# Performance work log

Measured on AMD Instinct MI355X. Metric: run time of the kernel, lower is better.

Reference implementation:

```python
import jax, jax.numpy as jnp
import numpy as np

D = 512
H = 8
HD = D // H
EPS = 1e-6


def layer_norm(x, a, b):
    # torch: std is unbiased (ddof=1); note division by (std + eps), not sqrt(var+eps)
    mean = x.mean(-1, keepdims=True)
    std = jnp.sqrt(x.var(-1, ddof=1, keepdims=True))
    return a * (x - mean) / (std + EPS) + b


def setup_inputs() -> dict:
    key = jax.random.key(0)
    ks = jax.random.split(key, 8)
    x = jax.random.normal(ks[0], (4, 2048, D), dtype=jnp.float32)
    s = 0.02
    return {
        "x": x,
        "ln1_a": jnp.ones((D,), jnp.float32),
        "ln1_b": jnp.zeros((D,), jnp.float32),
        "ln2_a": jnp.ones((D,), jnp.float32),
        "ln2_b": jnp.zeros((D,), jnp.float32),
        "wq": jax.random.normal(ks[1], (D, D), jnp.float32) * s,  # [out, in] torch layout
        "wk": jax.random.normal(ks[2], (D, D), jnp.float32) * s,
        "wv": jax.random.normal(ks[3], (D, D), jnp.float32) * s,
        "wo": jax.random.normal(ks[4], (D, D), jnp.float32) * s,
        "w1": jax.random.normal(ks[5], (D, D), jnp.float32) * s,  # MLP hidden == dim
        "b1": jnp.zeros((D,), jnp.float32),
        "w2": jax.random.normal(ks[6], (D, D), jnp.float32) * s,
        "b2": jnp.zeros((D,), jnp.float32),
    }


def reference(x, ln1_a, ln1_b, ln2_a, ln2_b, wq, wk, wv, wo, w1, b1, w2, b2):
    B, S, _ = x.shape
    xn = layer_norm(x, ln1_a, ln1_b)
    # attention (non-causal, dropout=identity in eval)
    q = (xn @ wq.T).reshape(B, S, H, HD)
    k = (xn @ wk.T).reshape(B, S, H, HD)
    v = (xn @ wv.T).reshape(B, S, H, HD)
    scores = jnp.einsum("bshd,bthd->bhst", q, k) / jnp.sqrt(jnp.float32(HD))
    probs = jax.nn.softmax(scores.astype(jnp.float32), axis=-1).astype(q.dtype)
    attn = jnp.einsum("bhst,bthd->bshd", probs, v).reshape(B, S, D)
    h = xn + attn @ wo.T
    # MLP
    hn = layer_norm(h, ln2_a, ln2_b)
    ffn = jax.nn.relu(hn @ w1.T + b1) @ w2.T + b2
    return h + ffn
```

## Files before the change

### kernel.cpp

```cpp
#include <hip/hip_runtime.h>


typedef short s16x8 __attribute__((ext_vector_type(8)));
typedef float f32x4 __attribute__((ext_vector_type(4)));
typedef unsigned short u16;
typedef u16 u16x4 __attribute__((ext_vector_type(4)));

__device__ __forceinline__ u16 f2b(float f) {
  union { float f; unsigned u; } c; c.f = f;
  return (u16)((c.u + 0x7FFFu + ((c.u >> 16) & 1u)) >> 16);
}

__device__ __forceinline__ f32x4 mfma16(s16x8 a, s16x8 b, f32x4 c) {
  return __builtin_amdgcn_mfma_f32_16x16x32_bf16(a, b, c, 0, 0, 0);
}

__device__ __forceinline__ void gload_lds16(const u16* g, u16* l) {
  __builtin_amdgcn_global_load_lds(
      (const __attribute__((address_space(1))) unsigned*)g,
      (__attribute__((address_space(3))) unsigned*)l, 16, 0, 0);
}

__global__ __launch_bounds__(256) void cast_w(
    const float* __restrict__ s0, const float* __restrict__ s1,
    const float* __restrict__ s2, const float* __restrict__ s3,
    const float* __restrict__ s4, const float* __restrict__ s5,
    u16* __restrict__ dst)
{
  int i = blockIdx.x * 256 + threadIdx.x;
  const float* s;
  switch (blockIdx.y) {
    case 0: s = s0; break; case 1: s = s1; break; case 2: s = s2; break;
    case 3: s = s3; break; case 4: s = s4; break; default: s = s5; break;
  }
  float4 v = ((const float4*)s)[i];
  u16x4 o; o.x = f2b(v.x); o.y = f2b(v.y); o.z = f2b(v.z); o.w = f2b(v.w);
  *(u16x4*)(dst + (size_t)blockIdx.y * 262144 + (size_t)i * 4) = o;
}

template<int OF, int OB>
__global__ __launch_bounds__(256) void ln_kernel(
    const float* __restrict__ x, const float* __restrict__ ga,
    const float* __restrict__ gbv, float* __restrict__ yf, u16* __restrict__ yb)
{
  int row = blockIdx.x * 4 + (threadIdx.x >> 6);
  int lane = threadIdx.x & 63;
  size_t base = (size_t)row * 512 + lane * 8;
  const float4* xr = (const float4*)(x + base);
  float4 v0 = xr[0], v1 = xr[1];
  float s  = v0.x + v0.y + v0.z + v0.w + v1.x + v1.y + v1.z + v1.w;
  float ss = v0.x*v0.x + v0.y*v0.y + v0.z*v0.z + v0.w*v0.w
           + v1.x*v1.x + v1.y*v1.y + v1.z*v1.z + v1.w*v1.w;
  #pragma unroll
  for (int m = 1; m < 64; m <<= 1) { s += __shfl_xor(s, m); ss += __shfl_xor(ss, m); }
  float mean = s * (1.0f / 512.0f);
  float var  = fmaxf((ss - 512.0f * mean * mean) * (1.0f / 511.0f), 0.0f);
  float inv  = 1.0f / (sqrtf(var) + 1e-6f);
  const float4* ap = (const float4*)(ga + lane * 8);
  const float4* bp = (const float4*)(gbv + lane * 8);
  float4 a0 = ap[0], a1 = ap[1], b0 = bp[0], b1 = bp[1];
  float4 y0, y1;
  y0.x = (v0.x-mean)*inv*a0.x + b0.x;  y0.y = (v0.y-mean)*inv*a0.y + b0.y;
  y0.z = (v0.z-mean)*inv*a0.z + b0.z;  y0.w = (v0.w-mean)*inv*a0.w + b0.w;
  y1.x = (v1.x-mean)*inv*a1.x + b1.x;  y1.y = (v1.y-mean)*inv*a1.y + b1.y;
  y1.z = (v1.z-mean)*inv*a1.z + b1.z;  y1.w = (v1.w-mean)*inv*a1.w + b1.w;
  if (OF) { float4* o = (float4*)(yf + base); o[0] = y0; o[1] = y1; }
  if (OB) {
    union { s16x8 v; u16 u[8]; } pk;
    pk.u[0]=f2b(y0.x); pk.u[1]=f2b(y0.y); pk.u[2]=f2b(y0.z); pk.u[3]=f2b(y0.w);
    pk.u[4]=f2b(y1.x); pk.u[5]=f2b(y1.y); pk.u[6]=f2b(y1.z); pk.u[7]=f2b(y1.w);
    *(s16x8*)(yb + base) = pk.v;
  }
}

template<int MODE>
__global__ __launch_bounds__(256) void gemm128(
    const u16* __restrict__ A, const u16* __restrict__ W,
    const float* __restrict__ bias, const float* __restrict__ resid,
    float* __restrict__ outf, u16* __restrict__ outb,
    u16* __restrict__ outb3, float qscale)
{
  __shared__ u16 als[2][128 * 32];
  __shared__ u16 bls[2][128 * 32];
  int t = threadIdx.x, lane = t & 63, w = t >> 6;
  int l15 = lane & 15, g = lane >> 4;
  int wr = w >> 1, wc = w & 1;
  int mbase = blockIdx.x * 128, nbase = blockIdx.y * 128;

  int r0 = t >> 2, cs = (t & 3) ^ ((r0 >> 1) & 3);
  size_t offA0 = (size_t)(mbase + r0) * 512 + cs * 8;
  size_t offA1 = (size_t)(mbase + r0 + 64) * 512 + cs * 8;
  size_t offB0 = (size_t)(nbase + r0) * 512 + cs * 8;
  size_t offB1 = (size_t)(nbase + r0 + 64) * 512 + cs * 8;

  #define GSTAGE(buf, k0) do {                                    \
    gload_lds16(A + (k0) + offA0, &als[buf][(w * 64) * 8]);       \
    gload_lds16(A + (k0) + offA1, &als[buf][(256 + w * 64) * 8]); \
    gload_lds16(W + (k0) + offB0, &bls[buf][(w * 64) * 8]);       \
    gload_lds16(W + (k0) + offB1, &bls[buf][(256 + w * 64) * 8]); \
  } while (0)

  int ar[4], br[4];
  #pragma unroll
  for (int i = 0; i < 4; ++i) {
    int rA = wr * 64 + i * 16 + l15;
    ar[i] = rA * 32 + ((g ^ ((rA >> 1) & 3)) << 3);
    int rB = wc * 64 + i * 16 + l15;
    br[i] = rB * 32 + ((g ^ ((rB >> 1) & 3)) << 3);
  }

  f32x4 zero = {0.0f, 0.0f, 0.0f, 0.0f};
  f32x4 acc[4][4];
  #pragma unroll
  for (int mi = 0; mi < 4; ++mi)
    #pragma unroll
    for (int ni = 0; ni < 4; ++ni) acc[mi][ni] = zero;

  GSTAGE(0, 0);
  __syncthreads();
  int cur = 0;
  for (int kk = 0; kk < 16; ++kk) {
    if (kk < 15) GSTAGE(cur ^ 1, (kk + 1) * 32);
    s16x8 af[4], bfr[4];
    #pragma unroll
    for (int i = 0; i < 4; ++i) {
      af[i]  = *(const s16x8*)&als[cur][ar[i]];
      bfr[i] = *(const s16x8*)&bls[cur][br[i]];
    }
    #pragma unroll
    for (int mi = 0; mi < 4; ++mi)
      #pragma unroll
      for (int ni = 0; ni < 4; ++ni)
        acc[mi][ni] = mfma16(af[mi], bfr[ni], acc[mi][ni]);
    __syncthreads();
    cur ^= 1;
  }
  #undef GSTAGE

  if (MODE & 128) {
    int bidx = mbase >> 11;
    int mb = mbase + wr * 64;
    #pragma unroll
    for (int ni = 0; ni < 4; ++ni) {
      int nn = nbase + wc * 64 + ni * 16 + l15;
      #pragma unroll
      for (int p = 0; p < 2; ++p) {
        int w32 = (mb + p * 32) & 2047;
        union { s16x8 v; u16 u[8]; } pkv;
        #pragma unroll
        for (int r = 0; r < 4; ++r) {
          pkv.u[2 * r]     = f2b(acc[2 * p][ni][r]);
          pkv.u[2 * r + 1] = f2b(acc[2 * p + 1][ni][r]);
        }
        *(s16x8*)(outb3 + ((size_t)bidx * 512 + nn) * 2048 + w32 + 8 * g) = pkv.v;
      }
    }
  } else {
    #pragma unroll
    for (int ni = 0; ni < 4; ++ni) {
      int n = nbase + wc * 64 + ni * 16 + l15;
      float bv = (MODE & 1) ? bias[n] : 0.0f;
      #pragma unroll
      for (int mi = 0; mi < 4; ++mi) {
        #pragma unroll
        for (int r = 0; r < 4; ++r) {
          int m = mbase + wr * 64 + mi * 16 + 4 * g + r;
          float v = acc[mi][ni][r] + bv;
          if (MODE & 2) v = fmaxf(v, 0.0f);
          if (MODE & 4) v += resid[(size_t)m * 512 + n];
          if (MODE & 8) outf[(size_t)m * 512 + n] = v;
          if (MODE & 16) {
            float vs = (MODE & 32) ? v * qscale : v;
            outb[(size_t)m * 512 + n] = f2b(vs);
          }
        }
      }
    }
  }
}

__global__ __launch_bounds__(256) void attn_kernel(
    const u16* __restrict__ q, const u16* __restrict__ k,
    const u16* __restrict__ vt, u16* __restrict__ o)
{
  __shared__ u16 kls[4][64 * 64];
  __shared__ u16 vls[4][64 * 64];
  int t = threadIdx.x, lane = t & 63, w = t >> 6;
  int l15 = lane & 15, g = lane >> 4;
  int sw = l15 & 7;
  int lrow = lane >> 3;
  int lchunk = (lane & 7) ^ (lrow & 7);
  int fid = blockIdx.x + 32 * blockIdx.y;
  int xcd = fid & 7, rest = fid >> 3;
  int bh = xcd * 4 + (rest & 3);
  int qt = rest >> 2;
  int bb = bh >> 3, h = bh & 7;
  int qbase = qt * 128 + w * 32;

  const u16* qp = q + (size_t)(bb * 2048 + qbase + l15) * 512 + h * 64 + g * 8;
  s16x8 qf0a = *(const s16x8*)qp;
  s16x8 qf1a = *(const s16x8*)(qp + 32);
  s16x8 qf0b = *(const s16x8*)(qp + 16 * 512);
  s16x8 qf1b = *(const s16x8*)(qp + 16 * 512 + 32);
  f32x4 zero = {0.0f, 0.0f, 0.0f, 0.0f};
  f32x4 oacc[2][4];
  #pragma unroll
  for (int qg = 0; qg < 2; ++qg)
    #pragma unroll
    for (int nf = 0; nf < 4; ++nf) oacc[qg][nf] = zero;
  float lsum[2] = {0.0f, 0.0f};
  const u16* kb0 = k + (size_t)(bb * 2048) * 512 + h * 64;
  const u16* vb0 = vt + (size_t)((bb * 8 + h) * 64) * 2048;

  #define STAGE(nb, tt) do {                                                  \
    int sr0 = w * 16 + lrow;                                                  \
    const u16* ks0 = kb0 + (size_t)((tt) * 64 + sr0) * 512 + lchunk * 8;      \
    const u16* vs0 = vb0 + (size_t)sr0 * 2048 + (tt) * 64 + lchunk * 8;       \
    gload_lds16(ks0, &kls[nb][(w * 16) * 64]);                                \
    gload_lds16(ks0 + (size_t)8 * 512, &kls[nb][(w * 16 + 8) * 64]);          \
    gload_lds16(vs0, &vls[nb][(w * 16) * 64]);                                \
    gload_lds16(vs0 + (size_t)8 * 2048, &vls[nb][(w * 16 + 8) * 64]);         \
  } while (0)

  #define QKT(kbuf, sdst) do {                                                \
    _Pragma("unroll")                                                         \
    for (int kg = 0; kg < 4; ++kg) {                                          \
      int rb = (kg * 16 + l15) * 64;                                          \
      s16x8 ka = *(const s16x8*)&(kbuf)[rb + ((g ^ sw) << 3)];                \
      s16x8 kc = *(const s16x8*)&(kbuf)[rb + (((4 + g) ^ sw) << 3)];          \
      sdst[0][kg] = mfma16(ka, qf0a, zero);                                   \
      sdst[0][kg] = mfma16(kc, qf1a, sdst[0][kg]);                            \
      sdst[1][kg] = mfma16(ka, qf0b, zero);                                   \
      sdst[1][kg] = mfma16(kc, qf1b, sdst[1][kg]);                            \
    }                                                                         \
  } while (0)

  #define SMAX(ssrc) do {                                                     \
    _Pragma("unroll")                                                         \
    for (int qg = 0; qg < 2; ++qg) {                                          \
      _Pragma("unroll")                                                       \
      for (int b2 = 0; b2 < 2; ++b2) {                                        \
        _Pragma("unroll")                                                     \
        for (int r = 0; r < 4; ++r) {                                         \
          float p0 = __builtin_amdgcn_exp2f(ssrc[qg][2 * b2][r]);             \
          float p1 = __builtin_amdgcn_exp2f(ssrc[qg][2 * b2 + 1][r]);         \
          lsum[qg] += p0 + p1;                                                \
          union { float f; unsigned u; } ua, ub;                              \
          ua.f = p0; ub.f = p1;                                               \
          pk[qg][b2].u32v[r] = __builtin_amdgcn_perm(ub.u, ua.u, 0x07060302u);\
        }                                                                     \
      }                                                                       \
    }                                                                         \
  } while (0)

  #define PVC(vbuf) do {                                                      \
    _Pragma("unroll")                                                         \
    for (int b2 = 0; b2 < 2; ++b2) {                                          \
      _Pragma("unroll")                                                       \
      for (int nf = 0; nf < 4; ++nf) {                                        \
        s16x8 vf = *(const s16x8*)                                            \
            &(vbuf)[(nf * 16 + l15) * 64 + ((((b2 << 2) | g) ^ sw) << 3)];    \
        oacc[0][nf] = mfma16(pk[0][b2].v8, vf, oacc[0][nf]);                  \
        oacc[1][nf] = mfma16(pk[1][b2].v8, vf, oacc[1][nf]);                  \
      }                                                                       \
    }                                                                         \
  } while (0)

  typedef union { s16x8 v8; unsigned u32v[4]; } pku;

  #define ITER(kt, scur, snxt) do {                                           \
    if ((kt) < 30) asm volatile("s_waitcnt vmcnt(4)" ::: "memory");           \
    else           asm volatile("s_waitcnt vmcnt(0)" ::: "memory");           \
    __builtin_amdgcn_s_barrier();                                             \
    if ((kt) + 3 < 32) STAGE(((kt) + 3) & 3, (kt) + 3);                       \
    if ((kt) + 1 < 32) QKT(kls[((kt) + 1) & 3], snxt);                        \
    pku pk[2][2];                                                             \
    SMAX(scur);                                                               \
    PVC(vls[(kt) & 3]);                                                       \
  } while (0)

  STAGE(0, 0);
  STAGE(1, 1);
  STAGE(2, 2);
  asm volatile("s_waitcnt vmcnt(8)" ::: "memory");
  __builtin_amdgcn_s_barrier();
  f32x4 sA[2][4], sB[2][4];
  QKT(kls[0], sA);

  for (int k2 = 0; k2 < 32; k2 += 2) {
    ITER(k2, sA, sB);
    ITER(k2 + 1, sB, sA);
  }
  #undef ITER
  #undef PVC
  #undef SMAX
  #undef QKT
  #undef STAGE

  #pragma unroll
  for (int qg = 0; qg < 2; ++qg) {
    float ls = lsum[qg];
    ls += __shfl_xor(ls, 16);
    ls += __shfl_xor(ls, 32);
    float linv = 1.0f / ls;
    size_t obase = (size_t)(bb * 2048 + qbase + qg * 16 + 4 * g) * 512
                 + h * 64 + l15;
    #pragma unroll
    for (int r = 0; r < 4; ++r) {
      float lr = __shfl(linv, 4 * g + r);
      #pragma unroll
      for (int nf = 0; nf < 4; ++nf)
        o[obase + (size_t)r * 512 + nf * 16] = f2b(oacc[qg][nf][r] * lr);
    }
  }
}

extern "C" void kernel_launch(void* const* d_in, const int* in_sizes, int n_in,
                              void* d_out, int out_size, void* d_ws, size_t ws_size,
                              hipStream_t stream)
{
  const float* x     = (const float*)d_in[0];
  const float* ln1_a = (const float*)d_in[1];
  const float* ln1_b = (const float*)d_in[2];
  const float* ln2_a = (const float*)d_in[3];
  const float* ln2_b = (const float*)d_in[4];
  const float* wq = (const float*)d_in[5];
  const float* wk = (const float*)d_in[6];
  const float* wv = (const float*)d_in[7];
  const float* wo = (const float*)d_in[8];
  const float* w1 = (const float*)d_in[9];
  const float* b1 = (const float*)d_in[10];
  const float* w2 = (const float*)d_in[11];
  const float* b2 = (const float*)d_in[12];

  char* ws = (char*)d_ws;
  float* xn_f = (float*)(ws + (size_t)0);
  float* h_f  = (float*)(ws + ((size_t)16 << 20));
  u16* xn_b = (u16*)(ws + ((size_t)32 << 20));
  u16* q_b  = (u16*)(ws + ((size_t)40 << 20));
  u16* k_b  = (u16*)(ws + ((size_t)48 << 20));
  u16* vt_b = (u16*)(ws + ((size_t)56 << 20));
  u16* at_b = (u16*)(ws + ((size_t)64 << 20));
  u16* wb   = (u16*)(ws + ((size_t)72 << 20));
  u16 *wkb = wb + 262144, *wvb = wb + 2 * 262144;
  u16 *wob = wb + 3 * 262144, *w1b = wb + 4 * 262144, *w2b = wb + 5 * 262144;
  u16* hn_b = q_b;
  u16* f_b  = at_b;

  dim3 blk(256);
  dim3 g512(64, 4);
  cast_w<<<dim3(256, 6), blk, 0, stream>>>(wq, wk, wv, wo, w1, w2, wb);
  ln_kernel<1, 1><<<dim3(2048), blk, 0, stream>>>(x, ln1_a, ln1_b, xn_f, xn_b);
  gemm128<16 | 32><<<g512, blk, 0, stream>>>(
      xn_b, wb, nullptr, nullptr, nullptr, q_b, nullptr, 0.18033688f);
  gemm128<16><<<g512, blk, 0, stream>>>(
      xn_b, wkb, nullptr, nullptr, nullptr, k_b, nullptr, 0.0f);
  gemm128<128><<<g512, blk, 0, stream>>>(
      xn_b, wvb, nullptr, nullptr, nullptr, nullptr, vt_b, 0.0f);
  attn_kernel<<<dim3(32, 16), blk, 0, stream>>>(q_b, k_b, vt_b, at_b);
  gemm128<4 | 8><<<g512, blk, 0, stream>>>(
      at_b, wob, nullptr, xn_f, h_f, nullptr, nullptr, 0.0f);
  ln_kernel<0, 1><<<dim3(2048), blk, 0, stream>>>(h_f, ln2_a, ln2_b, nullptr, hn_b);
  gemm128<1 | 2 | 16><<<g512, blk, 0, stream>>>(
      hn_b, w1b, b1, nullptr, nullptr, f_b, nullptr, 0.0f);
  gemm128<1 | 4 | 8><<<g512, blk, 0, stream>>>(
      f_b, w2b, b2, h_f, (float*)d_out, nullptr, nullptr, 0.0f);
}
```

Measured before the change: 141.9 us.

## Double GEMM K-tile to 64 with 8-way swizzle, add MFMA priority in attention

The GEMM now stages 64-wide K slices instead of 32, using an 8-chunk XOR swizzle. That halves the number of main-loop iterations and barriers per tile, at the cost of twice the LDS (64 KB per block), which may lower occupancy. The attention kernel raises wave priority around its QK^T and PV MFMA blocks with s_setprio so matrix work gets issued ahead of softmax. The Q/K/V projection launches are also reordered so V and K come before Q, probably to improve cache locality for the attention kernel.

After: 131.5 us. 1.08x faster.

```diff
diff --git a/kernel.cpp b/kernel.cpp
--- a/kernel.cpp
+++ b/kernel.cpp
@@ -80,33 +80,41 @@
     float* __restrict__ outf, u16* __restrict__ outb,
     u16* __restrict__ outb3, float qscale)
 {
-  __shared__ u16 als[2][128 * 32];
-  __shared__ u16 bls[2][128 * 32];
+  __shared__ u16 als[2][128 * 64];
+  __shared__ u16 bls[2][128 * 64];
   int t = threadIdx.x, lane = t & 63, w = t >> 6;
   int l15 = lane & 15, g = lane >> 4;
   int wr = w >> 1, wc = w & 1;
   int mbase = blockIdx.x * 128, nbase = blockIdx.y * 128;
 
-  int r0 = t >> 2, cs = (t & 3) ^ ((r0 >> 1) & 3);
-  size_t offA0 = (size_t)(mbase + r0) * 512 + cs * 8;
-  size_t offA1 = (size_t)(mbase + r0 + 64) * 512 + cs * 8;
-  size_t offB0 = (size_t)(nbase + r0) * 512 + cs * 8;
-  size_t offB1 = (size_t)(nbase + r0 + 64) * 512 + cs * 8;
-
-  #define GSTAGE(buf, k0) do {                                    \
-    gload_lds16(A + (k0) + offA0, &als[buf][(w * 64) * 8]);       \
-    gload_lds16(A + (k0) + offA1, &als[buf][(256 + w * 64) * 8]); \
-    gload_lds16(W + (k0) + offB0, &bls[buf][(w * 64) * 8]);       \
-    gload_lds16(W + (k0) + offB1, &bls[buf][(256 + w * 64) * 8]); \
-  } while (0)
-
-  int ar[4], br[4];
+  size_t offA[4], offB[4];
+  #pragma unroll
+  for (int j = 0; j < 4; ++j) {
+    int cid = j * 256 + t;
+    int row = cid >> 3, cs = (cid & 7) ^ (row & 7);
+    offA[j] = (size_t)(mbase + row) * 512 + cs * 8;
+    offB[j] = (size_t)(nbase + row) * 512 + cs * 8;
+  }
+
+  #define GSTAGE(buf, k0) do {                                        \
+    _Pragma("unroll")                                                 \
+    for (int j = 0; j < 4; ++j)                                       \
+      gload_lds16(A + (k0) + offA[j], &als[buf][(j * 256 + w * 64) * 8]); \
+    _Pragma("unroll")                                                 \
+    for (int j = 0; j < 4; ++j)                                       \
+      gload_lds16(W + (k0) + offB[j], &bls[buf][(j * 256 + w * 64) * 8]); \
+  } while (0)
+
+  int ar[4][2], br[4][2];
   #pragma unroll
   for (int i = 0; i < 4; ++i) {
     int rA = wr * 64 + i * 16 + l15;
-    ar[i] = rA * 32 + ((g ^ ((rA >> 1) & 3)) << 3);
     int rB = wc * 64 + i * 16 + l15;
-    br[i] = rB * 32 + ((g ^ ((rB >> 1) & 3)) << 3);
+    #pragma unroll
+    for (int kh = 0; kh < 2; ++kh) {
+      ar[i][kh] = rA * 64 + (((kh * 4 + g) ^ (rA & 7)) << 3);
+      br[i][kh] = rB * 64 + (((kh * 4 + g) ^ (rB & 7)) << 3);
+    }
   }
 
   f32x4 zero = {0.0f, 0.0f, 0.0f, 0.0f};
@@ -119,19 +127,24 @@
   GSTAGE(0, 0);
   __syncthreads();
   int cur = 0;
-  for (int kk = 0; kk < 16; ++kk) {
-    if (kk < 15) GSTAGE(cur ^ 1, (kk + 1) * 32);
-    s16x8 af[4], bfr[4];
+  for (int kk = 0; kk < 8; ++kk) {
+    if (kk < 7) GSTAGE(cur ^ 1, (kk + 1) * 64);
+    s16x8 af[4][2], bfr[4][2];
     #pragma unroll
     for (int i = 0; i < 4; ++i) {
-      af[i]  = *(const s16x8*)&als[cur][ar[i]];
-      bfr[i] = *(const s16x8*)&bls[cur][br[i]];
-    }
-    #pragma unroll
-    for (int mi = 0; mi < 4; ++mi)
-      #pragma unroll
-      for (int ni = 0; ni < 4; ++ni)
-        acc[mi][ni] = mfma16(af[mi], bfr[ni], acc[mi][ni]);
+      #pragma unroll
+      for (int kh = 0; kh < 2; ++kh) {
+        af[i][kh]  = *(const s16x8*)&als[cur][ar[i][kh]];
+        bfr[i][kh] = *(const s16x8*)&bls[cur][br[i][kh]];
+      }
+    }
+    #pragma unroll
+    for (int kh = 0; kh < 2; ++kh)
+      #pragma unroll
+      for (int mi = 0; mi < 4; ++mi)
+        #pragma unroll
+        for (int ni = 0; ni < 4; ++ni)
+          acc[mi][ni] = mfma16(af[mi][kh], bfr[ni][kh], acc[mi][ni]);
     __syncthreads();
     cur ^= 1;
   }
@@ -223,6 +236,7 @@
   } while (0)
 
   #define QKT(kbuf, sdst) do {                                                \
+    __builtin_amdgcn_s_setprio(1);                                            \
     _Pragma("unroll")                                                         \
     for (int kg = 0; kg < 4; ++kg) {                                          \
       int rb = (kg * 16 + l15) * 64;                                          \
@@ -233,6 +247,7 @@
       sdst[1][kg] = mfma16(ka, qf0b, zero);                                   \
       sdst[1][kg] = mfma16(kc, qf1b, sdst[1][kg]);                            \
     }                                                                         \
+    __builtin_amdgcn_s_setprio(0);                                            \
   } while (0)
 
   #define SMAX(ssrc) do {                                                     \
@@ -254,6 +269,7 @@
   } while (0)
 
   #define PVC(vbuf) do {                                                      \
+    __builtin_amdgcn_s_setprio(1);                                            \
     _Pragma("unroll")                                                         \
     for (int b2 = 0; b2 < 2; ++b2) {                                          \
       _Pragma("unroll")                                                       \
@@ -264,6 +280,7 @@
         oacc[1][nf] = mfma16(pk[1][b2].v8, vf, oacc[1][nf]);                  \
       }                                                                       \
     }                                                                         \
+    __builtin_amdgcn_s_setprio(0);                                            \
   } while (0)
 
   typedef union { s16x8 v8; unsigned u32v[4]; } pku;
@@ -351,12 +368,12 @@
   dim3 g512(64, 4);
   cast_w<<<dim3(256, 6), blk, 0, stream>>>(wq, wk, wv, wo, w1, w2, wb);
   ln_kernel<1, 1><<<dim3(2048), blk, 0, stream>>>(x, ln1_a, ln1_b, xn_f, xn_b);
+  gemm128<128><<<g512, blk, 0, stream>>>(
+      xn_b, wvb, nullptr, nullptr, nullptr, nullptr, vt_b, 0.0f);
+  gemm128<16><<<g512, blk, 0, stream>>>(
+      xn_b, wkb, nullptr, nullptr, nullptr, k_b, nullptr, 0.0f);
   gemm128<16 | 32><<<g512, blk, 0, stream>>>(
       xn_b, wb, nullptr, nullptr, nullptr, q_b, nullptr, 0.18033688f);
-  gemm128<16><<<g512, blk, 0, stream>>>(
-      xn_b, wkb, nullptr, nullptr, nullptr, k_b, nullptr, 0.0f);
-  gemm128<128><<<g512, blk, 0, stream>>>(
-      xn_b, wvb, nullptr, nullptr, nullptr, nullptr, vt_b, 0.0f);
   attn_kernel<<<dim3(32, 16), blk, 0, stream>>>(q_b, k_b, vt_b, at_b);
   gemm128<4 | 8><<<g512, blk, 0, stream>>>(
       at_b, wob, nullptr, xn_f, h_f, nullptr, nullptr, 0.0f);
```
